# Optimization experiments

Measured on AMD Instinct MI355X. Metric: run time of the kernel, lower is better.

## Reference

```python
import jax, jax.numpy as jnp
import numpy as np

B, MAXLEN = 256, 10000
N_ATOMS, N_BONDS, N_ANG, N_TOR = 2000, 1999, 1998, 1997
NBT, NAT, NTT = 50, 100, 200
EPS = 1e-8


def setup_inputs() -> dict:
    rng = np.random.default_rng(0)
    feats = np.zeros((B, MAXLEN, 9), np.float32)
    # col 0: atom types
    feats[:, :N_ATOMS, 0] = rng.integers(0, 20, (B, N_ATOMS))
    # col 5: flattened coords [3*N]
    coords = (rng.standard_normal((B, N_ATOMS, 3)) * 2.0).astype(np.float32)
    feats[:, :3 * N_ATOMS, 5] = coords.reshape(B, -1)
    # col 6: bonds (i, j, type) along a chain
    i = np.arange(N_BONDS, dtype=np.float32)
    bonds = np.zeros((B, N_BONDS, 3), np.float32)
    bonds[..., 0] = i; bonds[..., 1] = i + 1
    bonds[..., 2] = rng.integers(0, NBT, (B, N_BONDS))
    feats[:, :3 * N_BONDS, 6] = bonds.reshape(B, -1)
    # col 7: angles (i, j, k, type)
    a = np.arange(N_ANG, dtype=np.float32)
    angs = np.zeros((B, N_ANG, 4), np.float32)
    angs[..., 0] = a; angs[..., 1] = a + 1; angs[..., 2] = a + 2
    angs[..., 3] = rng.integers(0, NAT, (B, N_ANG))
    feats[:, :4 * N_ANG, 7] = angs.reshape(B, -1)
    # col 8: torsions (i, j, k, l, type)
    t = np.arange(N_TOR, dtype=np.float32)
    tors = np.zeros((B, N_TOR, 5), np.float32)
    tors[..., 0] = t; tors[..., 1] = t + 1; tors[..., 2] = t + 2; tors[..., 3] = t + 3
    tors[..., 4] = rng.integers(0, NTT, (B, N_TOR))
    feats[:, :5 * N_TOR, 8] = tors.reshape(B, -1)
    # per-column valid lengths
    lengths = np.zeros((B, 9), np.int32)
    lengths[:, 0] = N_ATOMS
    lengths[:, 5] = 3 * N_ATOMS
    lengths[:, 6] = 3 * N_BONDS
    lengths[:, 7] = 4 * N_ANG
    lengths[:, 8] = 5 * N_TOR
    # learned params: (k, eq_value, multiplicity) per type row
    P = NBT + NAT + NTT
    opt = np.abs(rng.standard_normal((P, 3))).astype(np.float32)
    opt[:, 2] = rng.integers(1, 4, P).astype(np.float32)
    return {
        "features": jnp.asarray(feats),
        "lengths": jnp.asarray(lengths),
        "opt_pars": jnp.asarray(opt),
        "bond_type": jnp.arange(NBT, dtype=jnp.float32),
        "angle_type": jnp.arange(NAT, dtype=jnp.float32) + NBT,
        "tor_type": jnp.arange(NTT, dtype=jnp.float32) + NBT + NAT,
    }


def _gather(coords, idx):
    # coords [B,N,3], idx [B,M] -> [B,M,3]
    return jnp.take_along_axis(
        coords, jnp.broadcast_to(idx[..., None], idx.shape + (3,)), axis=1)


def _energy(features, lengths, opt_pars, bond_map, angle_map, tor_map):
    Bn = features.shape[0]
    coords = features[:, :3 * N_ATOMS, 5].reshape(Bn, N_ATOMS, 3)
    bonds = features[:, :3 * N_BONDS, 6].reshape(Bn, N_BONDS, 3).astype(jnp.int32)
    angs = features[:, :4 * N_ANG, 7].reshape(Bn, N_ANG, 4).astype(jnp.int32)
    tors = features[:, :5 * N_TOR, 8].reshape(Bn, N_TOR, 5).astype(jnp.int32)

    # ---- bonds: harmonic E = k * (r - r0)^2 ----
    ri, rj = _gather(coords, bonds[..., 0]), _gather(coords, bonds[..., 1])
    r = jnp.sqrt(jnp.sum((ri - rj) ** 2, -1) + EPS)          # [B,NB]
    pb = opt_pars[bond_map[bonds[..., 2]]]                   # [B,NB,3]
    eb = pb[..., 0] * (r - pb[..., 1]) ** 2
    mb = jnp.arange(N_BONDS)[None, :] < (lengths[:, 6:7] // 3)
    ebonds = jnp.sum(jnp.where(mb, eb, 0.0), -1)

    # ---- angles: harmonic E = k * (theta - theta0)^2 ----
    ai, aj, ak = (_gather(coords, angs[..., c]) for c in range(3))
    u, v = ai - aj, ak - aj
    cos = jnp.sum(u * v, -1) * jax.lax.rsqrt(
        (jnp.sum(u * u, -1) + EPS) * (jnp.sum(v * v, -1) + EPS))
    theta = jnp.arccos(jnp.clip(cos, -1.0 + 1e-6, 1.0 - 1e-6))
    pa = opt_pars[angle_map[angs[..., 3]]]
    ea = pa[..., 0] * (theta - pa[..., 1]) ** 2
    ma = jnp.arange(N_ANG)[None, :] < (lengths[:, 7:8] // 4)
    eangles = jnp.sum(jnp.where(ma, ea, 0.0), -1)

    # ---- torsions: E = k * (1 + cos(n*phi - phi0)) ----
    ti, tj, tk, tl = (_gather(coords, tors[..., c]) for c in range(4))
    b1, b2, b3 = tj - ti, tk - tj, tl - tk
    n1 = jnp.cross(b1, b2)
    n2 = jnp.cross(b2, b3)
    b2h = b2 * jax.lax.rsqrt(jnp.sum(b2 * b2, -1, keepdims=True) + EPS)
    m1 = jnp.cross(n1, b2h)
    phi = jnp.arctan2(jnp.sum(m1 * n2, -1), jnp.sum(n1 * n2, -1))
    pt = opt_pars[tor_map[tors[..., 4]]]
    et = pt[..., 0] * (1.0 + jnp.cos(pt[..., 2] * phi - pt[..., 1]))
    mt = jnp.arange(N_TOR)[None, :] < (lengths[:, 8:9] // 5)
    etors = jnp.sum(jnp.where(mt, et, 0.0), -1)

    return ebonds + eangles + etors                          # [B]


def reference(features, lengths, opt_pars, bond_type, angle_type, tor_type):
    return _energy(features, lengths, opt_pars,
                   bond_type.astype(jnp.int32),
                   angle_type.astype(jnp.int32),
                   tor_type.astype(jnp.int32))
```

## Files before the change

### kernel.cpp

```cpp
#include <hip/hip_runtime.h>


#define EBS 1024

constexpr int BATCH  = 256;
constexpr int MAXLEN = 10000;
constexpr int NBT = 50, NAT = 100, NTT = 200;
constexpr float EPS = 1e-8f;

constexpr int OFF_SC  = 0;
constexpr int OFF_SBP = OFF_SC  + 6000 * 4;
constexpr int OFF_SAP = OFF_SBP + 150 * 4;
constexpr int OFF_STP = OFF_SAP + 300 * 4;
constexpr int OFF_SW  = OFF_STP + 600 * 4;
constexpr int OFF_SB  = OFF_SW  + 16 * 4;
constexpr int OFF_SA  = OFF_SB  + 6000 * 2;
constexpr int OFF_ST  = OFF_SA  + 8000 * 2;
constexpr int SMEM_BYTES = OFF_ST + 10000 * 2;

__global__ __launch_bounds__(EBS) void energy_kernel(
    const float* __restrict__ features,
    const int*   __restrict__ lengths,
    const float* __restrict__ opt_pars,
    const float* __restrict__ bond_type,
    const float* __restrict__ angle_type,
    const float* __restrict__ tor_type,
    float*       __restrict__ out)
{
    extern __shared__ char smem[];
    float*          sc  = (float*)(smem + OFF_SC);
    float*          sbp = (float*)(smem + OFF_SBP);
    float*          sap = (float*)(smem + OFF_SAP);
    float*          stp = (float*)(smem + OFF_STP);
    float*          sw  = (float*)(smem + OFF_SW);
    unsigned short* sb  = (unsigned short*)(smem + OFF_SB);
    unsigned short* sa  = (unsigned short*)(smem + OFF_SA);
    unsigned short* st  = (unsigned short*)(smem + OFF_ST);

    const int b   = blockIdx.x;
    const int tid = threadIdx.x;
    const float* __restrict__ fb = features + (size_t)b * MAXLEN * 9;

    for (int i = tid; i < NBT; i += EBS) {
        int idx = (int)bond_type[i];
        sbp[3*i+0] = opt_pars[3*idx+0];
        sbp[3*i+1] = opt_pars[3*idx+1];
        sbp[3*i+2] = opt_pars[3*idx+2];
    }
    for (int i = tid; i < NAT; i += EBS) {
        int idx = (int)angle_type[i];
        sap[3*i+0] = opt_pars[3*idx+0];
        sap[3*i+1] = opt_pars[3*idx+1];
        sap[3*i+2] = opt_pars[3*idx+2];
    }
    for (int i = tid; i < NTT; i += EBS) {
        int idx = (int)tor_type[i];
        stp[3*i+0] = opt_pars[3*idx+0];
        stp[3*i+1] = opt_pars[3*idx+1];
        stp[3*i+2] = opt_pars[3*idx+2];
    }

    #pragma unroll 2
    for (int i = tid; i < MAXLEN; i += EBS) {
        const float* __restrict__ row = fb + 9 * i + 5;
        float vc = row[0];
        float vb = row[1];
        float va = row[2];
        float vt = row[3];
        if (i < 6000)  sc[i] = vc;
        if (i < 6000)  sb[i] = (unsigned short)(int)vb;
        if (i < 8000)  sa[i] = (unsigned short)(int)va;
        st[i] = (unsigned short)(int)vt;
    }
    __syncthreads();

    float acc = 0.0f;

    {
        const int nb = lengths[b * 9 + 6] / 3;
        for (int t = tid; t < nb; t += EBS) {
            int i  = sb[3*t+0];
            int j  = sb[3*t+1];
            int ty = sb[3*t+2];
            float dx = sc[3*i+0] - sc[3*j+0];
            float dy = sc[3*i+1] - sc[3*j+1];
            float dz = sc[3*i+2] - sc[3*j+2];
            float r  = sqrtf(dx*dx + dy*dy + dz*dz + EPS);
            float k  = sbp[3*ty+0];
            float d  = r - sbp[3*ty+1];
            acc += k * d * d;
        }
    }

    {
        const int na = lengths[b * 9 + 7] / 4;
        for (int t = tid; t < na; t += EBS) {
            int i  = sa[4*t+0];
            int j  = sa[4*t+1];
            int k_ = sa[4*t+2];
            int ty = sa[4*t+3];
            float jx = sc[3*j+0], jy = sc[3*j+1], jz = sc[3*j+2];
            float ux = sc[3*i+0] - jx, uy = sc[3*i+1] - jy, uz = sc[3*i+2] - jz;
            float vx = sc[3*k_+0] - jx, vy = sc[3*k_+1] - jy, vz = sc[3*k_+2] - jz;
            float uv = ux*vx + uy*vy + uz*vz;
            float uu = ux*ux + uy*uy + uz*uz;
            float vv = vx*vx + vy*vy + vz*vz;
            float cth = uv * rsqrtf((uu + EPS) * (vv + EPS));
            cth = fminf(fmaxf(cth, -1.0f + 1e-6f), 1.0f - 1e-6f);
            float theta = acosf(cth);
            float k  = sap[3*ty+0];
            float d  = theta - sap[3*ty+1];
            acc += k * d * d;
        }
    }

    {
        const int nt = lengths[b * 9 + 8] / 5;
        for (int t = tid; t < nt; t += EBS) {
            int i  = st[5*t+0];
            int j  = st[5*t+1];
            int k_ = st[5*t+2];
            int l  = st[5*t+3];
            int ty = st[5*t+4];
            float ix = sc[3*i+0],  iy = sc[3*i+1],  iz = sc[3*i+2];
            float jx = sc[3*j+0],  jy = sc[3*j+1],  jz = sc[3*j+2];
            float kx = sc[3*k_+0], ky = sc[3*k_+1], kz = sc[3*k_+2];
            float lx = sc[3*l+0],  ly = sc[3*l+1],  lz = sc[3*l+2];
            float b1x = jx - ix, b1y = jy - iy, b1z = jz - iz;
            float b2x = kx - jx, b2y = ky - jy, b2z = kz - jz;
            float b3x = lx - kx, b3y = ly - ky, b3z = lz - kz;
            float n1x = b1y*b2z - b1z*b2y;
            float n1y = b1z*b2x - b1x*b2z;
            float n1z = b1x*b2y - b1y*b2x;
            float n2x = b2y*b3z - b2z*b3y;
            float n2y = b2z*b3x - b2x*b3z;
            float n2z = b2x*b3y - b2y*b3x;
            float inv = rsqrtf(b2x*b2x + b2y*b2y + b2z*b2z + EPS);
            float hx = b2x * inv, hy = b2y * inv, hz = b2z * inv;
            float m1x = n1y*hz - n1z*hy;
            float m1y = n1z*hx - n1x*hz;
            float m1z = n1x*hy - n1y*hx;
            float sy = m1x*n2x + m1y*n2y + m1z*n2z;
            float sx = n1x*n2x + n1y*n2y + n1z*n2z;
            float phi = atan2f(sy, sx);
            float k  = stp[3*ty+0];
            float p0 = stp[3*ty+1];
            float n  = stp[3*ty+2];
            acc += k * (1.0f + cosf(n * phi - p0));
        }
    }

    for (int off = 32; off > 0; off >>= 1)
        acc += __shfl_down(acc, off, 64);
    const int wave = tid >> 6, lane = tid & 63;
    if (lane == 0) sw[wave] = acc;
    __syncthreads();
    if (tid == 0) {
        float v = 0.0f;
        #pragma unroll
        for (int w = 0; w < EBS / 64; ++w) v += sw[w];
        out[b] = v;
    }
}

extern "C" void kernel_launch(void* const* d_in, const int* in_sizes, int n_in,
                              void* d_out, int out_size, void* d_ws, size_t ws_size,
                              hipStream_t stream) {
    const float* features   = (const float*)d_in[0];
    const int*   lengths    = (const int*)  d_in[1];
    const float* opt_pars   = (const float*)d_in[2];
    const float* bond_type  = (const float*)d_in[3];
    const float* angle_type = (const float*)d_in[4];
    const float* tor_type   = (const float*)d_in[5];
    float* out = (float*)d_out;

    hipFuncSetAttribute((const void*)energy_kernel,
                        hipFuncAttributeMaxDynamicSharedMemorySize, SMEM_BYTES);

    const int B = out_size;
    energy_kernel<<<B, EBS, SMEM_BYTES, stream>>>(
        features, lengths, opt_pars, bond_type, angle_type, tor_type, out);
}
```

Measured before the change: 148.7 us.

## Split each batch row into four slices with halo and a second reduce kernel

Each batch item now goes to four 512-thread blocks. Each block loads only its 2500-row slice of the features, plus a small halo, into static shared memory, and computes the bonds, angles and torsions whose records start inside that slice. Coordinates that fall outside the slice are read directly from global memory. Partial sums are written to the workspace and combined by a small second kernel. The aim is to raise block count and occupancy by cutting shared memory per block and to stop each block reading the whole row, at the cost of an extra launch and some uncoalesced global fallback reads.

```diff
diff --git a/kernel.cpp b/kernel.cpp
--- a/kernel.cpp
+++ b/kernel.cpp
@@ -1,90 +1,97 @@
 #include <hip/hip_runtime.h>
 
 
-#define EBS 1024
-
-constexpr int BATCH  = 256;
+#define PBS 512
+#define SLICES 4
+#define RPS 2500
+#define HALO 12
+#define SL (RPS + HALO)
+
 constexpr int MAXLEN = 10000;
 constexpr int NBT = 50, NAT = 100, NTT = 200;
 constexpr float EPS = 1e-8f;
 
-constexpr int OFF_SC  = 0;
-constexpr int OFF_SBP = OFF_SC  + 6000 * 4;
-constexpr int OFF_SAP = OFF_SBP + 150 * 4;
-constexpr int OFF_STP = OFF_SAP + 300 * 4;
-constexpr int OFF_SW  = OFF_STP + 600 * 4;
-constexpr int OFF_SB  = OFF_SW  + 16 * 4;
-constexpr int OFF_SA  = OFF_SB  + 6000 * 2;
-constexpr int OFF_ST  = OFF_SA  + 8000 * 2;
-constexpr int SMEM_BYTES = OFF_ST + 10000 * 2;
-
-__global__ __launch_bounds__(EBS) void energy_kernel(
+__global__ __launch_bounds__(PBS) void partial_kernel(
     const float* __restrict__ features,
     const int*   __restrict__ lengths,
     const float* __restrict__ opt_pars,
     const float* __restrict__ bond_type,
     const float* __restrict__ angle_type,
     const float* __restrict__ tor_type,
-    float*       __restrict__ out)
+    float*       __restrict__ part)
 {
-    extern __shared__ char smem[];
-    float*          sc  = (float*)(smem + OFF_SC);
-    float*          sbp = (float*)(smem + OFF_SBP);
-    float*          sap = (float*)(smem + OFF_SAP);
-    float*          stp = (float*)(smem + OFF_STP);
-    float*          sw  = (float*)(smem + OFF_SW);
-    unsigned short* sb  = (unsigned short*)(smem + OFF_SB);
-    unsigned short* sa  = (unsigned short*)(smem + OFF_SA);
-    unsigned short* st  = (unsigned short*)(smem + OFF_ST);
-
-    const int b   = blockIdx.x;
+    __shared__ float          scoord[SL];
+    __shared__ float          sbp[3 * NBT];
+    __shared__ float          sap[3 * NAT];
+    __shared__ float          stp[3 * NTT];
+    __shared__ float          sw[PBS / 64];
+    __shared__ unsigned short sbond[SL];
+    __shared__ unsigned short sang[SL];
+    __shared__ unsigned short stor[SL];
+
+    const int blk = blockIdx.x;
+    const int b   = blk >> 2;
+    const int s   = blk & (SLICES - 1);
+    const int r0  = s * RPS;
+    const int r1  = r0 + RPS;
     const int tid = threadIdx.x;
     const float* __restrict__ fb = features + (size_t)b * MAXLEN * 9;
 
-    for (int i = tid; i < NBT; i += EBS) {
+    for (int i = tid; i < NBT; i += PBS) {
         int idx = (int)bond_type[i];
         sbp[3*i+0] = opt_pars[3*idx+0];
         sbp[3*i+1] = opt_pars[3*idx+1];
         sbp[3*i+2] = opt_pars[3*idx+2];
     }
-    for (int i = tid; i < NAT; i += EBS) {
+    for (int i = tid; i < NAT; i += PBS) {
         int idx = (int)angle_type[i];
         sap[3*i+0] = opt_pars[3*idx+0];
         sap[3*i+1] = opt_pars[3*idx+1];
         sap[3*i+2] = opt_pars[3*idx+2];
     }
-    for (int i = tid; i < NTT; i += EBS) {
+    for (int i = tid; i < NTT; i += PBS) {
         int idx = (int)tor_type[i];
         stp[3*i+0] = opt_pars[3*idx+0];
         stp[3*i+1] = opt_pars[3*idx+1];
         stp[3*i+2] = opt_pars[3*idx+2];
     }
 
-    #pragma unroll 2
-    for (int i = tid; i < MAXLEN; i += EBS) {
-        const float* __restrict__ row = fb + 9 * i + 5;
-        float vc = row[0];
-        float vb = row[1];
-        float va = row[2];
-        float vt = row[3];
-        if (i < 6000)  sc[i] = vc;
-        if (i < 6000)  sb[i] = (unsigned short)(int)vb;
-        if (i < 8000)  sa[i] = (unsigned short)(int)va;
-        st[i] = (unsigned short)(int)vt;
+    {
+        const int iend = min(MAXLEN, r1 + HALO);
+        for (int i = r0 + tid; i < iend; i += PBS) {
+            const float* __restrict__ row = fb + 9 * i + 5;
+            float vc = row[0];
+            float vb = row[1];
+            float va = row[2];
+            float vt = row[3];
+            const int li = i - r0;
+            if (i < 6000) scoord[li] = vc;
+            if (i < 5997) sbond[li] = (unsigned short)(int)vb;
+            if (i < 7992) sang[li]  = (unsigned short)(int)va;
+            if (i < 9985) stor[li]  = (unsigned short)(int)vt;
+        }
     }
     __syncthreads();
 
+    auto getc = [&](int g) -> float {
+        unsigned li = (unsigned)(g - r0);
+        return (li < (unsigned)SL) ? scoord[li] : fb[9 * g + 5];
+    };
+
     float acc = 0.0f;
 
     {
         const int nb = lengths[b * 9 + 6] / 3;
-        for (int t = tid; t < nb; t += EBS) {
-            int i  = sb[3*t+0];
-            int j  = sb[3*t+1];
-            int ty = sb[3*t+2];
-            float dx = sc[3*i+0] - sc[3*j+0];
-            float dy = sc[3*i+1] - sc[3*j+1];
-            float dz = sc[3*i+2] - sc[3*j+2];
+        const int tb = (r0 + 2) / 3;
+        const int te = min(nb, (r1 + 2) / 3);
+        for (int t = tb + tid; t < te; t += PBS) {
+            const int f0 = 3 * t - r0;
+            int i  = sbond[f0];
+            int j  = sbond[f0 + 1];
+            int ty = sbond[f0 + 2];
+            float dx = getc(3*i+0) - getc(3*j+0);
+            float dy = getc(3*i+1) - getc(3*j+1);
+            float dz = getc(3*i+2) - getc(3*j+2);
             float r  = sqrtf(dx*dx + dy*dy + dz*dz + EPS);
             float k  = sbp[3*ty+0];
             float d  = r - sbp[3*ty+1];
@@ -94,14 +101,17 @@
 
     {
         const int na = lengths[b * 9 + 7] / 4;
-        for (int t = tid; t < na; t += EBS) {
-            int i  = sa[4*t+0];
-            int j  = sa[4*t+1];
-            int k_ = sa[4*t+2];
-            int ty = sa[4*t+3];
-            float jx = sc[3*j+0], jy = sc[3*j+1], jz = sc[3*j+2];
-            float ux = sc[3*i+0] - jx, uy = sc[3*i+1] - jy, uz = sc[3*i+2] - jz;
-            float vx = sc[3*k_+0] - jx, vy = sc[3*k_+1] - jy, vz = sc[3*k_+2] - jz;
+        const int ab = (r0 + 3) / 4;
+        const int ae = min(na, (r1 + 3) / 4);
+        for (int a = ab + tid; a < ae; a += PBS) {
+            const int f0 = 4 * a - r0;
+            int i  = sang[f0];
+            int j  = sang[f0 + 1];
+            int k_ = sang[f0 + 2];
+            int ty = sang[f0 + 3];
+            float jx = getc(3*j+0), jy = getc(3*j+1), jz = getc(3*j+2);
+            float ux = getc(3*i+0) - jx, uy = getc(3*i+1) - jy, uz = getc(3*i+2) - jz;
+            float vx = getc(3*k_+0) - jx, vy = getc(3*k_+1) - jy, vz = getc(3*k_+2) - jz;
             float uv = ux*vx + uy*vy + uz*vz;
             float uu = ux*ux + uy*uy + uz*uz;
             float vv = vx*vx + vy*vy + vz*vz;
@@ -116,16 +126,19 @@
 
     {
         const int nt = lengths[b * 9 + 8] / 5;
-        for (int t = tid; t < nt; t += EBS) {
-            int i  = st[5*t+0];
-            int j  = st[5*t+1];
-            int k_ = st[5*t+2];
-            int l  = st[5*t+3];
-            int ty = st[5*t+4];
-            float ix = sc[3*i+0],  iy = sc[3*i+1],  iz = sc[3*i+2];
-            float jx = sc[3*j+0],  jy = sc[3*j+1],  jz = sc[3*j+2];
-            float kx = sc[3*k_+0], ky = sc[3*k_+1], kz = sc[3*k_+2];
-            float lx = sc[3*l+0],  ly = sc[3*l+1],  lz = sc[3*l+2];
+        const int tb = (r0 + 4) / 5;
+        const int te = min(nt, (r1 + 4) / 5);
+        for (int t = tb + tid; t < te; t += PBS) {
+            const int f0 = 5 * t - r0;
+            int i  = stor[f0];
+            int j  = stor[f0 + 1];
+            int k_ = stor[f0 + 2];
+            int l  = stor[f0 + 3];
+            int ty = stor[f0 + 4];
+            float ix = getc(3*i+0),  iy = getc(3*i+1),  iz = getc(3*i+2);
+            float jx = getc(3*j+0),  jy = getc(3*j+1),  jz = getc(3*j+2);
+            float kx = getc(3*k_+0), ky = getc(3*k_+1), kz = getc(3*k_+2);
+            float lx = getc(3*l+0),  ly = getc(3*l+1),  lz = getc(3*l+2);
             float b1x = jx - ix, b1y = jy - iy, b1z = jz - iz;
             float b2x = kx - jx, b2y = ky - jy, b2z = kz - jz;
             float b3x = lx - kx, b3y = ly - ky, b3z = lz - kz;
@@ -158,7 +171,19 @@
     if (tid == 0) {
         float v = 0.0f;
         #pragma unroll
-        for (int w = 0; w < EBS / 64; ++w) v += sw[w];
+        for (int w = 0; w < PBS / 64; ++w) v += sw[w];
+        part[blk] = v;
+    }
+}
+
+__global__ __launch_bounds__(256) void reduce_kernel(
+    const float* __restrict__ part, float* __restrict__ out, int B)
+{
+    int b = blockIdx.x * 256 + threadIdx.x;
+    if (b < B) {
+        float v = 0.0f;
+        #pragma unroll
+        for (int i = 0; i < SLICES; ++i) v += part[b * SLICES + i];
         out[b] = v;
     }
 }
@@ -172,12 +197,11 @@
     const float* bond_type  = (const float*)d_in[3];
     const float* angle_type = (const float*)d_in[4];
     const float* tor_type   = (const float*)d_in[5];
-    float* out = (float*)d_out;
-
-    hipFuncSetAttribute((const void*)energy_kernel,
-                        hipFuncAttributeMaxDynamicSharedMemorySize, SMEM_BYTES);
+    float* out  = (float*)d_out;
+    float* part = (float*)d_ws;
 
     const int B = out_size;
-    energy_kernel<<<B, EBS, SMEM_BYTES, stream>>>(
-        features, lengths, opt_pars, bond_type, angle_type, tor_type, out);
+    partial_kernel<<<B * SLICES, PBS, 0, stream>>>(
+        features, lengths, opt_pars, bond_type, angle_type, tor_type, part);
+    reduce_kernel<<<(B + 255) / 256, 256, 0, stream>>>(part, out, B);
 }
```

Result: slower. 160.2 us (+7.8%).

## Stage feature rows through shared memory with coalesced float4 loads and prefetch

Applied to the files above, without the earlier changes.

Replaces the strided per-row global reads of the 9-float feature rows with fully coalesced float4 loads of 1024-row chunks into a shared-memory staging buffer. The next chunk is prefetched into registers while the current one is unpacked into the coordinate and index arrays. The aim is to cut wasted global bandwidth from reading only 4 of 9 floats per row with a stride-36-byte pattern. In exchange it reads all 9 columns, roughly doubling the bytes fetched, and adds two block barriers per chunk plus about 37KB more LDS.

```diff
diff --git a/kernel.cpp b/kernel.cpp
--- a/kernel.cpp
+++ b/kernel.cpp
@@ -3,12 +3,17 @@
 
 #define EBS 1024
 
-constexpr int BATCH  = 256;
 constexpr int MAXLEN = 10000;
 constexpr int NBT = 50, NAT = 100, NTT = 200;
 constexpr float EPS = 1e-8f;
 
-constexpr int OFF_SC  = 0;
+constexpr int CHUNK_ROWS = 1024;
+constexpr int CHUNK_F4   = CHUNK_ROWS * 9 / 4;
+constexpr int NCHUNK     = (MAXLEN + CHUNK_ROWS - 1) / CHUNK_ROWS;
+constexpr int SYS_F4     = MAXLEN * 9 / 4;
+
+constexpr int OFF_RAW = 0;
+constexpr int OFF_SC  = OFF_RAW + CHUNK_F4 * 16;
 constexpr int OFF_SBP = OFF_SC  + 6000 * 4;
 constexpr int OFF_SAP = OFF_SBP + 150 * 4;
 constexpr int OFF_STP = OFF_SAP + 300 * 4;
@@ -27,19 +32,22 @@
     const float* __restrict__ tor_type,
     float*       __restrict__ out)
 {
-    extern __shared__ char smem[];
-    float*          sc  = (float*)(smem + OFF_SC);
-    float*          sbp = (float*)(smem + OFF_SBP);
-    float*          sap = (float*)(smem + OFF_SAP);
-    float*          stp = (float*)(smem + OFF_STP);
-    float*          sw  = (float*)(smem + OFF_SW);
-    unsigned short* sb  = (unsigned short*)(smem + OFF_SB);
-    unsigned short* sa  = (unsigned short*)(smem + OFF_SA);
-    unsigned short* st  = (unsigned short*)(smem + OFF_ST);
+    extern __shared__ __align__(16) char smem[];
+    float4*         raw4 = (float4*)(smem + OFF_RAW);
+    float*          rawf = (float*)(smem + OFF_RAW);
+    float*          sc   = (float*)(smem + OFF_SC);
+    float*          sbp  = (float*)(smem + OFF_SBP);
+    float*          sap  = (float*)(smem + OFF_SAP);
+    float*          stp  = (float*)(smem + OFF_STP);
+    float*          sw   = (float*)(smem + OFF_SW);
+    unsigned short* sb   = (unsigned short*)(smem + OFF_SB);
+    unsigned short* sa   = (unsigned short*)(smem + OFF_SA);
+    unsigned short* st   = (unsigned short*)(smem + OFF_ST);
 
     const int b   = blockIdx.x;
     const int tid = threadIdx.x;
-    const float* __restrict__ fb = features + (size_t)b * MAXLEN * 9;
+    const float4* __restrict__ fv =
+        (const float4*)(features + (size_t)b * MAXLEN * 9);
 
     for (int i = tid; i < NBT; i += EBS) {
         int idx = (int)bond_type[i];
@@ -60,19 +68,44 @@
         stp[3*i+2] = opt_pars[3*idx+2];
     }
 
-    #pragma unroll 2
-    for (int i = tid; i < MAXLEN; i += EBS) {
-        const float* __restrict__ row = fb + 9 * i + 5;
-        float vc = row[0];
-        float vb = row[1];
-        float va = row[2];
-        float vt = row[3];
-        if (i < 6000)  sc[i] = vc;
-        if (i < 6000)  sb[i] = (unsigned short)(int)vb;
-        if (i < 8000)  sa[i] = (unsigned short)(int)va;
-        st[i] = (unsigned short)(int)vt;
-    }
-    __syncthreads();
+    float4 pre0, pre1, pre2;
+    const float4 zero4 = make_float4(0.f, 0.f, 0.f, 0.f);
+
+    auto load_chunk = [&](int ck) {
+        const int base = ck * CHUNK_F4;
+        const int i0 = base + tid;
+        const int i1 = base + tid + 1024;
+        const int i2 = base + tid + 2048;
+        pre0 = (i0 < SYS_F4) ? fv[i0] : zero4;
+        pre1 = (i1 < SYS_F4) ? fv[i1] : zero4;
+        pre2 = (tid < CHUNK_F4 - 2048 && i2 < SYS_F4) ? fv[i2] : zero4;
+    };
+    auto write_chunk = [&]() {
+        raw4[tid]        = pre0;
+        raw4[tid + 1024] = pre1;
+        if (tid < CHUNK_F4 - 2048) raw4[tid + 2048] = pre2;
+    };
+
+    load_chunk(0);
+    for (int ck = 0; ck < NCHUNK; ++ck) {
+        write_chunk();
+        __syncthreads();
+        if (ck + 1 < NCHUNK) load_chunk(ck + 1);
+        {
+            const int r = ck * CHUNK_ROWS + tid;
+            if (r < MAXLEN) {
+                const int o = 9 * tid + 5;
+                float vc = rawf[o + 0];
+                float vb = rawf[o + 1];
+                float va = rawf[o + 2];
+                float vt = rawf[o + 3];
+                if (r < 6000) { sc[r] = vc; sb[r] = (unsigned short)(int)vb; }
+                if (r < 8000) sa[r] = (unsigned short)(int)va;
+                st[r] = (unsigned short)(int)vt;
+            }
+        }
+        __syncthreads();
+    }
 
     float acc = 0.0f;
 
```

Result: no change. 151.1 us (+1.6%).
